# Kernel tuning notes

Hardware: AMD Instinct MI355X
Metric: run time of the kernel (lower is better)

## Reference

```python
import jax, jax.numpy as jnp
from jax import lax
import numpy as np

SCALE_N = 4
KERN = 5
PAD = KERN // 2
_G = np.float32([[0.003765, 0.015019, 0.023792, 0.015019, 0.003765],
                 [0.015019, 0.059912, 0.094907, 0.059912, 0.015019],
                 [0.023792, 0.094907, 0.150342, 0.094907, 0.023792],
                 [0.015019, 0.059912, 0.094907, 0.059912, 0.015019],
                 [0.003765, 0.015019, 0.023792, 0.015019, 0.003765]])
FILTER = jnp.asarray(_G)


def _lap_split(img):
    N, c, H, W = img.shape
    f = jnp.broadcast_to(FILTER, (c, 1, KERN, KERN))
    smooth = lax.conv_general_dilated(img, f, (1, 1), [(PAD, PAD), (PAD, PAD)],
                                      feature_group_count=c)
    lo = smooth[:, :, ::2, ::2]
    oph, opw = (H + 1) % 2, (W + 1) % 2
    # conv_transpose2d(stride=2, padding=PAD, output_padding) as lhs-dilated conv
    # (Gaussian kernel is symmetric, so no spatial flip needed)
    lo2 = 4.0 * lax.conv_general_dilated(
        lo, f, (1, 1),
        [(KERN - 1 - PAD, KERN - 1 - PAD + oph), (KERN - 1 - PAD, KERN - 1 - PAD + opw)],
        lhs_dilation=(2, 2), feature_group_count=c)
    hi = img - lo2
    return lo, hi


def _pyramid(img):
    levels = []
    for _ in range(SCALE_N):
        img, hi = _lap_split(img)
        levels.append(hi)
    levels.append(img)
    return levels


def _sample_points(img, xs, ys):
    # bilinear grid_sample, align_corners=False, zero padding.
    # img: (N,C,H,W); xs, ys: (P,) normalized coords in [-1,1]. -> (N,C,P)
    N, C, H, W = img.shape
    fx = ((xs + 1.0) * W - 1.0) * 0.5
    fy = ((ys + 1.0) * H - 1.0) * 0.5
    x0 = jnp.floor(fx)
    y0 = jnp.floor(fy)
    wx = fx - x0
    wy = fy - y0
    x0i = x0.astype(jnp.int32)
    y0i = y0.astype(jnp.int32)
    out = jnp.zeros((N, C, xs.shape[0]), img.dtype)
    corners = [(0, 0, (1 - wx) * (1 - wy)), (1, 0, wx * (1 - wy)),
               (0, 1, (1 - wx) * wy), (1, 1, wx * wy)]
    for dx, dy, w in corners:
        xc = x0i + dx
        yc = y0i + dy
        valid = (xc >= 0) & (xc < W) & (yc >= 0) & (yc < H)
        xcc = jnp.clip(xc, 0, W - 1)
        ycc = jnp.clip(yc, 0, H - 1)
        vals = img[:, :, ycc, xcc]  # (N,C,P) gather
        out = out + vals * (w * valid)[None, None, :]
    return out


def setup_inputs() -> dict:
    key = jax.random.key(0)
    k1, k2, k3 = jax.random.split(key, 3)
    N, c, H, W = 64, 32, 128, 128
    outdims = 4096
    m = SCALE_N + 1
    x = jax.random.normal(k1, (N, c, H, W), dtype=jnp.float32)
    grid = jax.random.uniform(k2, (1, outdims, 1, 2), minval=-0.1, maxval=0.1,
                              dtype=jnp.float32)
    features = (jnp.full((1, m * c, 1, outdims), 1.0 / c, jnp.float32)
                + 0.01 * jax.random.normal(k3, (1, m * c, 1, outdims), jnp.float32))
    bias = jnp.zeros((outdims,), jnp.float32)
    return {"x": x, "grid": grid, "features": features, "bias": bias}


def reference(x, grid, features, bias):
    N, c, H, W = x.shape
    m = SCALE_N + 1
    outdims = grid.shape[1]
    g = jnp.clip(grid, -1.0, 1.0)
    xs = g[0, :, 0, 0]  # width coord
    ys = g[0, :, 0, 1]  # height coord
    levels = _pyramid(x)
    pools = [_sample_points(lv, xs, ys) for lv in levels]  # each (N,c,P)
    y = jnp.concatenate(pools, axis=1)  # (N, m*c, P)
    feat = features.reshape(1, m * c, outdims)
    y = (y * feat).sum(axis=1)  # (N, P)
    return y + bias
```

## Files before the change

kernel.cpp:

```cpp
#include <hip/hip_runtime.h>
#include <hip/hip_fp16.h>


#define P1 66
#define P2 34
#define P3 18
#define P4 10
#define OFF_LO1 0
#define OFF_LO2 4224
#define OFF_LO3 5312
#define OFF_LO4 5600
#define SLOT    5680
#define SLOT4   1420

#define G_A 0.0613609f
#define G_B 0.2447700f
#define G_C 0.3877386f

#define T_FOFF   16384
#define PYR_FOFF 196608
#define PSTRIDE  5696

static __device__ __forceinline__ float clampf(float v, float lo, float hi) {
    return fminf(fmaxf(v, lo), hi);
}
static __device__ __forceinline__ int imin(int a, int b) { return a < b ? a : b; }
static __device__ __forceinline__ int imax(int a, int b) { return a > b ? a : b; }

static __device__ __forceinline__ unsigned int pack_h2(float a, float b) {
    __half ha = __float2half_rn(a), hb = __float2half_rn(b);
    unsigned short ua = *(unsigned short*)&ha, ub = *(unsigned short*)&hb;
    return (unsigned int)ua | ((unsigned int)ub << 16);
}
static __device__ __forceinline__ unsigned int pack_u2(int a, int b) {
    return (unsigned int)(a & 0xffff) | ((unsigned int)b << 16);
}
static __device__ __forceinline__ float2 uph2(unsigned int u) {
    unsigned short lo = (unsigned short)(u & 0xffff), hi = (unsigned short)(u >> 16);
    __half hl = *(__half*)&lo, hh = *(__half*)&hi;
    return make_float2(__half2float(hl), __half2float(hh));
}

__global__ void init_out_kernel(const float* __restrict__ bias, float* __restrict__ y) {
    int i = blockIdx.x * blockDim.x + threadIdx.x;
    y[i] = bias[i & 4095];
}

__global__ void weights_kernel(const float* __restrict__ grid, float* __restrict__ ws) {
    int out = blockIdx.x * blockDim.x + threadIdx.x;
    if (out >= 4096) return;
    float xs = clampf(grid[2 * out + 0], -1.f, 1.f);
    float ys = clampf(grid[2 * out + 1], -1.f, 1.f);

    uint4* L0 = (uint4*)ws;
    uint2* T  = (uint2*)(ws + T_FOFF);

    float fx = (xs + 1.f) * 64.f - 0.5f;
    float fy = (ys + 1.f) * 64.f - 0.5f;
    float x0f = floorf(fx), y0f = floorf(fy);
    int x0 = (int)x0f, y0 = (int)y0f;
    float wx = fx - x0f, wy = fy - y0f;
    float ux0 = (x0 >= 0)      ? (1.f - wx) : 0.f;
    float ux1 = (x0 + 1 < 128) ? wx         : 0.f;
    float uy0 = (y0 >= 0)      ? (1.f - wy) : 0.f;
    float uy1 = (y0 + 1 < 128) ? wy         : 0.f;
    int cx0 = imax(x0, 0), cx1 = imin(x0 + 1, 127);
    int cy0 = imax(y0, 0), cy1 = imin(y0 + 1, 127);
    L0[out] = make_uint4(pack_h2(ux0 * uy0, ux1 * uy0),
                         pack_h2(ux0 * uy1, ux1 * uy1),
                         pack_u2(cy0 * 128 + cx0, cy0 * 128 + cx1),
                         pack_u2(cy1 * 128 + cx0, cy1 * 128 + cx1));

    int   x0p = x0, y0p = y0;
    float ux0p = ux0, ux1p = ux1, uy0p = uy0, uy1p = uy1;

    const int offs[4]    = {OFF_LO1, OFF_LO2, OFF_LO3, OFF_LO4};
    const int strides[4] = {P1, P2, P3, P4};

    for (int j = 1; j <= 4; ++j) {
        const int Wj = 128 >> j, Pj = strides[j - 1], off = offs[j - 1];

        int qx; float a0, a1, a2;
        if (x0p & 1) { qx = (x0p - 1) >> 1;
            a0 = G_B * ux0p + G_A * ux1p; a1 = G_B * ux0p + G_C * ux1p; a2 = G_A * ux1p; }
        else         { qx = (x0p >> 1) - 1;
            a0 = G_A * ux0p; a1 = G_C * ux0p + G_B * ux1p; a2 = G_A * ux0p + G_B * ux1p; }
        int qy; float e0, e1, e2;
        if (y0p & 1) { qy = (y0p - 1) >> 1;
            e0 = G_B * uy0p + G_A * uy1p; e1 = G_B * uy0p + G_C * uy1p; e2 = G_A * uy1p; }
        else         { qy = (y0p >> 1) - 1;
            e0 = G_A * uy0p; e1 = G_C * uy0p + G_B * uy1p; e2 = G_A * uy0p + G_B * uy1p; }

        float half = (float)(Wj >> 1);
        float fxj = (xs + 1.f) * half - 0.5f;
        float fyj = (ys + 1.f) * half - 0.5f;
        float x0jf = floorf(fxj), y0jf = floorf(fyj);
        int x0j = (int)x0jf, y0j = (int)y0jf;
        float wxj = fxj - x0jf, wyj = fyj - y0jf;
        float ux0j = (x0j >= 0)     ? (1.f - wxj) : 0.f;
        float ux1j = (x0j + 1 < Wj) ? wxj         : 0.f;
        float uy0j = (y0j >= 0)     ? (1.f - wyj) : 0.f;
        float uy1j = (y0j + 1 < Wj) ? wyj         : 0.f;

        int bxb = qx & ~1;
        bxb = imin(imax(bxb, 0), Wj - 4);

        float axv[4], bxv[4], ayv[3], byv[3];
        int rv[3];
#pragma unroll
        for (int t = 0; t < 4; ++t) {
            int col = bxb + t;
            int s = col - qx;
            float av = (s == 0) ? a0 : (s == 1) ? a1 : (s == 2) ? a2 : 0.f;
            if (s < 0 || s > 2) av = 0.f;
            int sb = col - x0j;
            float bv = (sb == 0) ? ux0j : (sb == 1) ? ux1j : 0.f;
            axv[t] = av;
            bxv[t] = bv;
        }
#pragma unroll
        for (int t = 0; t < 3; ++t) {
            int row = qy + t;
            bool v = (row >= 0) && (row < Wj);
            float av = (t == 0) ? e0 : (t == 1) ? e1 : e2;
            ayv[t] = v ? av : 0.f;
            int sb = row - y0j;
            byv[t] = (sb == 0) ? uy0j : (sb == 1) ? uy1j : 0.f;
            int rc = imin(imax(row, 0), Wj - 1);
            rv[t] = off + rc * Pj + bxb;
        }

        int tb = (j - 1) * 5 * 4096 + out;
        T[tb]            = make_uint2(pack_h2(axv[0], axv[1]), pack_h2(axv[2], axv[3]));
        T[tb + 4096]     = make_uint2(pack_h2(bxv[0], bxv[1]), pack_h2(bxv[2], bxv[3]));
        T[tb + 2 * 4096] = make_uint2(pack_h2(ayv[0], ayv[1]), pack_h2(ayv[2], 0.f));
        T[tb + 3 * 4096] = make_uint2(pack_h2(byv[0], byv[1]), pack_h2(byv[2], 0.f));
        T[tb + 4 * 4096] = make_uint2(pack_u2(rv[0], rv[1]), pack_u2(rv[2], 0));

        x0p = x0j; y0p = y0j;
        ux0p = ux0j; ux1p = ux1j; uy0p = uy0j; uy1p = uy1j;
    }
}

static __device__ __forceinline__ float down_pt_lds(const float* s, int stride, int S,
                                                    int i, int j) {
    const float g1[5] = {G_A, G_B, G_C, G_B, G_A};
    int by = 2 * i - 2, bx = 2 * j - 2;
    float acc = 0.f;
    if (by >= 0 && by + 4 < S && bx >= 0 && bx + 4 < S) {
#pragma unroll
        for (int dy = 0; dy < 5; ++dy) {
            const float* r = s + (by + dy) * stride + bx;
            acc += g1[dy] * (G_A * (r[0] + r[4]) + G_B * (r[1] + r[3]) + G_C * r[2]);
        }
    } else {
#pragma unroll
        for (int dy = 0; dy < 5; ++dy) {
            int yy = by + dy;
            if ((unsigned)yy < (unsigned)S) {
#pragma unroll
                for (int dx = 0; dx < 5; ++dx) {
                    int xx = bx + dx;
                    if ((unsigned)xx < (unsigned)S)
                        acc += g1[dy] * g1[dx] * s[yy * stride + xx];
                }
            }
        }
    }
    return acc;
}

static __device__ __forceinline__ void build_pyramid(const float* __restrict__ img,
                                                     float* __restrict__ s_lo, int tid) {
    const float g1[5] = {G_A, G_B, G_C, G_B, G_A};

    for (int r = tid; r < 1024; r += 256) {
        int i = r >> 4, j0 = (r & 15) << 2;
        int by = 2 * i - 2;
        float acc[4] = {0.f, 0.f, 0.f, 0.f};
        if (i >= 1 && i <= 62 && j0 >= 4 && j0 <= 56) {
            const int a = 2 * j0 - 4;
#pragma unroll
            for (int dy = 0; dy < 5; ++dy) {
                const float* rp = img + (by + dy) * 128 + a;
                float4 q0 = *(const float4*)(rp);
                float4 q1 = *(const float4*)(rp + 4);
                float4 q2 = *(const float4*)(rp + 8);
                float4 q3 = *(const float4*)(rp + 12);
                float s2 = q0.z, s3 = q0.w, s4 = q1.x, s5 = q1.y, s6 = q1.z,
                      s7 = q1.w, s8 = q2.x, s9 = q2.y, s10 = q2.z, s11 = q2.w,
                      s12 = q3.x;
                float g = g1[dy];
                acc[0] += g * (G_A * (s2 + s6)  + G_B * (s3 + s5)  + G_C * s4);
                acc[1] += g * (G_A * (s4 + s8)  + G_B * (s5 + s7)  + G_C * s6);
                acc[2] += g * (G_A * (s6 + s10) + G_B * (s7 + s9)  + G_C * s8);
                acc[3] += g * (G_A * (s8 + s12) + G_B * (s9 + s11) + G_C * s10);
            }
        } else {
            int bx = 2 * j0 - 2;
#pragma unroll
            for (int dy = 0; dy < 5; ++dy) {
                int yy = by + dy;
                if ((unsigned)yy < 128u) {
#pragma unroll
                    for (int t = 0; t < 11; ++t) {
                        int xx = bx + t;
                        if ((unsigned)xx < 128u) {
                            float v = img[yy * 128 + xx];
#pragma unroll
                            for (int jj = 0; jj < 4; ++jj) {
                                int dx = t - 2 * jj;
                                if (dx >= 0 && dx <= 4) acc[jj] += g1[dy] * g1[dx] * v;
                            }
                        }
                    }
                }
            }
        }
        int base = OFF_LO1 + i * P1 + j0;
        *(float2*)&s_lo[base]     = make_float2(acc[0], acc[1]);
        *(float2*)&s_lo[base + 2] = make_float2(acc[2], acc[3]);
    }
    __syncthreads();

    for (int p = tid; p < 1024; p += 256) {
        int i = p >> 5, j = p & 31;
        s_lo[OFF_LO2 + i * P2 + j] = down_pt_lds(s_lo + OFF_LO1, P1, 64, i, j);
    }
    __syncthreads();

    {
        int i = tid >> 4, j = tid & 15;
        s_lo[OFF_LO3 + i * P3 + j] = down_pt_lds(s_lo + OFF_LO2, P2, 32, i, j);
    }
    __syncthreads();

    if (tid < 64) {
        int i = tid >> 3, j = tid & 7;
        s_lo[OFF_LO4 + i * P4 + j] = down_pt_lds(s_lo + OFF_LO3, P3, 16, i, j);
    }
    __syncthreads();
}

__global__ __launch_bounds__(256) void pyr_build_kernel(
    const float* __restrict__ x, float* __restrict__ ws)
{
    __shared__ __align__(16) float s_lo[SLOT];
    const int tid = threadIdx.x;
    const int bid = blockIdx.x;
    const float* img = x + ((size_t)bid << 14);

    build_pyramid(img, s_lo, tid);

    float4* g4 = (float4*)(ws + PYR_FOFF + (size_t)bid * PSTRIDE);
    const float4* s4 = (const float4*)s_lo;
    for (int i = tid; i < SLOT4; i += 256) g4[i] = s4[i];
}

__global__ __launch_bounds__(256) void pyr_gather_kernel(
    const float* __restrict__ x, const float* __restrict__ wrec,
    const float* __restrict__ feat, const float* __restrict__ bias,
    float* __restrict__ y)
{
    __shared__ __align__(16) float s_p[2][PSTRIDE];
    const int tid  = threadIdx.x;
    const int n    = blockIdx.x >> 4;
    const int tile = blockIdx.x & 15;
    const int out  = (tile << 8) + tid;

    const uint4* L0 = (const uint4*)wrec;
    const uint2* T  = (const uint2*)(wrec + T_FOFF);

    uint4 h0 = L0[out];
    float2 wA = uph2(h0.x), wB = uph2(h0.y);
    int o00 = (int)(h0.z & 0xffff), o01 = (int)(h0.z >> 16);
    int o10 = (int)(h0.w & 0xffff), o11 = (int)(h0.w >> 16);

    float ax[4][4], bx[4][4], ay[4][3], by[4][3];
    int   rv[4][3];
#pragma unroll
    for (int j = 0; j < 4; ++j) {
        const int tb = j * 5 * 4096 + out;
        uint2 uAX = T[tb];
        uint2 uBX = T[tb + 4096];
        uint2 uAY = T[tb + 2 * 4096];
        uint2 uBY = T[tb + 3 * 4096];
        uint2 uR  = T[tb + 4 * 4096];
        float2 t;
        t = uph2(uAX.x); ax[j][0] = t.x; ax[j][1] = t.y;
        t = uph2(uAX.y); ax[j][2] = t.x; ax[j][3] = t.y;
        t = uph2(uBX.x); bx[j][0] = t.x; bx[j][1] = t.y;
        t = uph2(uBX.y); bx[j][2] = t.x; bx[j][3] = t.y;
        t = uph2(uAY.x); ay[j][0] = t.x; ay[j][1] = t.y;
        ay[j][2] = uph2(uAY.y).x;
        t = uph2(uBY.x); by[j][0] = t.x; by[j][1] = t.y;
        by[j][2] = uph2(uBY.y).x;
        rv[j][0] = (int)(uR.x & 0xffff);
        rv[j][1] = (int)(uR.x >> 16);
        rv[j][2] = (int)(uR.y & 0xffff);
    }

    const float* img_n = x + ((size_t)n << 19);
    const float* pyr_n = wrec + PYR_FOFF + (size_t)n * 32 * PSTRIDE;

    {
        const float4* g = (const float4*)pyr_n;
        float4* d = (float4*)s_p[0];
        for (int i = tid; i < SLOT4; i += 256) d[i] = g[i];
    }
    __syncthreads();

    float acc = 0.f;
#pragma unroll 1
    for (int c = 0; c < 32; ++c) {
        const int cur = c & 1;

        float4 st0, st1, st2, st3, st4, st5;
        const bool have_next = (c + 1 < 32);
        if (have_next) {
            const float4* g = (const float4*)(pyr_n + (size_t)(c + 1) * PSTRIDE);
            int i0 = tid;
            st0 = g[i0];
            st1 = g[i0 + 256];
            st2 = g[i0 + 512];
            st3 = g[i0 + 768];
            st4 = g[i0 + 1024];
            st5 = (i0 + 1280 < SLOT4) ? g[i0 + 1280] : make_float4(0.f, 0.f, 0.f, 0.f);
        }

        const float* sl  = s_p[cur];
        const float* img = img_n + ((size_t)c << 14);
        float f_prev = feat[((size_t)c << 12) + out];
        float v0 = wA.x * img[o00] + wA.y * img[o01] + wB.x * img[o10] + wB.y * img[o11];
        float a = f_prev * v0;

#pragma unroll
        for (int j = 0; j < 4; ++j) {
            float f_cur = feat[((size_t)((j + 1) * 32 + c) << 12) + out];
            int r0 = rv[j][0], r1 = rv[j][1], r2 = rv[j][2];
            float2 p0a = *(const float2*)(sl + r0);
            float2 p0b = *(const float2*)(sl + r0 + 2);
            float2 p1a = *(const float2*)(sl + r1);
            float2 p1b = *(const float2*)(sl + r1 + 2);
            float2 p2a = *(const float2*)(sl + r2);
            float2 p2b = *(const float2*)(sl + r2 + 2);
            float ra0 = ax[j][0] * p0a.x + ax[j][1] * p0a.y + ax[j][2] * p0b.x + ax[j][3] * p0b.y;
            float ra1 = ax[j][0] * p1a.x + ax[j][1] * p1a.y + ax[j][2] * p1b.x + ax[j][3] * p1b.y;
            float ra2 = ax[j][0] * p2a.x + ax[j][1] * p2a.y + ax[j][2] * p2b.x + ax[j][3] * p2b.y;
            float rb0 = bx[j][0] * p0a.x + bx[j][1] * p0a.y + bx[j][2] * p0b.x + bx[j][3] * p0b.y;
            float rb1 = bx[j][0] * p1a.x + bx[j][1] * p1a.y + bx[j][2] * p1b.x + bx[j][3] * p1b.y;
            float rb2 = bx[j][0] * p2a.x + bx[j][1] * p2a.y + bx[j][2] * p2b.x + bx[j][3] * p2b.y;
            float sa = ay[j][0] * ra0 + ay[j][1] * ra1 + ay[j][2] * ra2;
            float sb = by[j][0] * rb0 + by[j][1] * rb1 + by[j][2] * rb2;
            a += f_cur * sb - 4.f * f_prev * sa;
            f_prev = f_cur;
        }
        acc += a;

        if (have_next) {
            float4* d = (float4*)s_p[cur ^ 1];
            int i0 = tid;
            d[i0]        = st0;
            d[i0 + 256]  = st1;
            d[i0 + 512]  = st2;
            d[i0 + 768]  = st3;
            d[i0 + 1024] = st4;
            if (i0 + 1280 < SLOT4) d[i0 + 1280] = st5;
        }
        __syncthreads();
    }

    y[((size_t)n << 12) + out] = acc + bias[out];
}

__global__ __launch_bounds__(256, 3) void pyr_sample_fused(
    const float* __restrict__ x, const float* __restrict__ wrec,
    const float* __restrict__ feat, float* __restrict__ y)
{
    __shared__ __align__(16) float s_lo[SLOT];
    const int tid = threadIdx.x;
    const int n   = blockIdx.x >> 5;
    const int c   = blockIdx.x & 31;
    const float* img = x + ((size_t)(n * 32 + c) << 14);

    build_pyramid(img, s_lo, tid);

    const uint4* L0 = (const uint4*)wrec;
    const uint2* T  = (const uint2*)(wrec + T_FOFF);
    float* yrow = y + ((size_t)n << 12);
    for (int out = tid; out < 4096; out += 256) {
        uint4 h0 = L0[out];
        float2 wA = uph2(h0.x), wB = uph2(h0.y);
        int o00 = (int)(h0.z & 0xffff), o01 = (int)(h0.z >> 16);
        int o10 = (int)(h0.w & 0xffff), o11 = (int)(h0.w >> 16);

        float f_prev = feat[((size_t)c << 12) + out];
        float v0 = wA.x * img[o00] + wA.y * img[o01] + wB.x * img[o10] + wB.y * img[o11];
        float acc = f_prev * v0;

#pragma unroll
        for (int j = 1; j <= 4; ++j) {
            const int tb = (j - 1) * 5 * 4096 + out;
            uint2 uAX = T[tb];
            uint2 uBX = T[tb + 4096];
            uint2 uAY = T[tb + 2 * 4096];
            uint2 uBY = T[tb + 3 * 4096];
            uint2 uR  = T[tb + 4 * 4096];
            float2 ax01 = uph2(uAX.x), ax23 = uph2(uAX.y);
            float2 bx01 = uph2(uBX.x), bx23 = uph2(uBX.y);
            float2 ay01 = uph2(uAY.x); float ay2 = uph2(uAY.y).x;
            float2 by01 = uph2(uBY.x); float by2 = uph2(uBY.y).x;
            int r0 = (int)(uR.x & 0xffff), r1 = (int)(uR.x >> 16), r2 = (int)(uR.y & 0xffff);

            float f_cur = feat[((size_t)(j * 32 + c) << 12) + out];

            float2 p0a = *(const float2*)&s_lo[r0];
            float2 p0b = *(const float2*)&s_lo[r0 + 2];
            float2 p1a = *(const float2*)&s_lo[r1];
            float2 p1b = *(const float2*)&s_lo[r1 + 2];
            float2 p2a = *(const float2*)&s_lo[r2];
            float2 p2b = *(const float2*)&s_lo[r2 + 2];
            float ra0 = ax01.x * p0a.x + ax01.y * p0a.y + ax23.x * p0b.x + ax23.y * p0b.y;
            float ra1 = ax01.x * p1a.x + ax01.y * p1a.y + ax23.x * p1b.x + ax23.y * p1b.y;
            float ra2 = ax01.x * p2a.x + ax01.y * p2a.y + ax23.x * p2b.x + ax23.y * p2b.y;
            float rb0 = bx01.x * p0a.x + bx01.y * p0a.y + bx23.x * p0b.x + bx23.y * p0b.y;
            float rb1 = bx01.x * p1a.x + bx01.y * p1a.y + bx23.x * p1b.x + bx23.y * p1b.y;
            float rb2 = bx01.x * p2a.x + bx01.y * p2a.y + bx23.x * p2b.x + bx23.y * p2b.y;
            float sa = ay01.x * ra0 + ay01.y * ra1 + ay2 * ra2;
            float sb = by01.x * rb0 + by01.y * rb1 + by2 * rb2;
            acc += f_cur * sb - 4.f * f_prev * sa;
            f_prev = f_cur;
        }
        atomicAdd(&yrow[out], acc);
    }
}

extern "C" void kernel_launch(void* const* d_in, const int* in_sizes, int n_in,
                              void* d_out, int out_size, void* d_ws, size_t ws_size,
                              hipStream_t stream) {
    (void)in_sizes; (void)n_in;
    const float* x    = (const float*)d_in[0];
    const float* grid = (const float*)d_in[1];
    const float* feat = (const float*)d_in[2];
    const float* bias = (const float*)d_in[3];
    float* y  = (float*)d_out;
    float* ws = (float*)d_ws;

    const size_t NEED = sizeof(float) * ((size_t)PYR_FOFF + 2048ull * PSTRIDE);

    weights_kernel<<<16, 256, 0, stream>>>(grid, ws);
    if (ws_size >= NEED) {
        pyr_build_kernel<<<2048, 256, 0, stream>>>(x, ws);
        pyr_gather_kernel<<<1024, 256, 0, stream>>>(x, ws, feat, bias, y);
    } else {
        init_out_kernel<<<out_size / 256, 256, 0, stream>>>(bias, y);
        pyr_sample_fused<<<2048, 256, 0, stream>>>(x, ws, feat, y);
    }
}
```

Measured before the change: 365.3 us.

## Compute 4 output rows per thread in level-1 blur with separable row reuse

Each thread now computes a 4x4 block of the first downsampled level instead of looping over 1x4 quads. It does the horizontal 5-tap filter once per input row and reuses it across the vertical taps of the four output rows, so an 11-row window is read instead of 20. The gather kernel's block index is also swizzled to change the order in which images and tiles are scheduled across CUs. The cost is more accumulator registers per thread, which may lower occupancy.

```diff
diff --git a/kernel.cpp b/kernel.cpp
--- a/kernel.cpp
+++ b/kernel.cpp
@@ -170,56 +170,81 @@
     return acc;
 }
 
-static __device__ __forceinline__ void build_pyramid(const float* __restrict__ img,
-                                                     float* __restrict__ s_lo, int tid) {
+static __device__ __forceinline__ void border_quad(const float* __restrict__ img,
+                                                   int i, int j0, float acc[4]) {
     const float g1[5] = {G_A, G_B, G_C, G_B, G_A};
-
-    for (int r = tid; r < 1024; r += 256) {
-        int i = r >> 4, j0 = (r & 15) << 2;
-        int by = 2 * i - 2;
-        float acc[4] = {0.f, 0.f, 0.f, 0.f};
-        if (i >= 1 && i <= 62 && j0 >= 4 && j0 <= 56) {
+    int by = 2 * i - 2, bx = 2 * j0 - 2;
+#pragma unroll
+    for (int dy = 0; dy < 5; ++dy) {
+        int yy = by + dy;
+        if ((unsigned)yy < 128u) {
+#pragma unroll
+            for (int t = 0; t < 11; ++t) {
+                int xx = bx + t;
+                if ((unsigned)xx < 128u) {
+                    float v = img[yy * 128 + xx];
+#pragma unroll
+                    for (int jj = 0; jj < 4; ++jj) {
+                        int dx = t - 2 * jj;
+                        if (dx >= 0 && dx <= 4) acc[jj] += g1[dy] * g1[dx] * v;
+                    }
+                }
+            }
+        }
+    }
+}
+
+static __device__ __forceinline__ void build_pyramid1(const float* __restrict__ img,
+                                                      float* __restrict__ s_lo, int tid) {
+    const float g1[5] = {G_A, G_B, G_C, G_B, G_A};
+
+    {
+        const int jq = tid & 15;
+        const int s  = tid >> 4;
+        const int j0 = jq << 2;
+        float acc[4][4] = {{0.f,0.f,0.f,0.f},{0.f,0.f,0.f,0.f},
+                           {0.f,0.f,0.f,0.f},{0.f,0.f,0.f,0.f}};
+        if (jq >= 1 && jq <= 14) {
             const int a = 2 * j0 - 4;
-#pragma unroll
-            for (int dy = 0; dy < 5; ++dy) {
-                const float* rp = img + (by + dy) * 128 + a;
-                float4 q0 = *(const float4*)(rp);
-                float4 q1 = *(const float4*)(rp + 4);
-                float4 q2 = *(const float4*)(rp + 8);
-                float4 q3 = *(const float4*)(rp + 12);
-                float s2 = q0.z, s3 = q0.w, s4 = q1.x, s5 = q1.y, s6 = q1.z,
-                      s7 = q1.w, s8 = q2.x, s9 = q2.y, s10 = q2.z, s11 = q2.w,
-                      s12 = q3.x;
-                float g = g1[dy];
-                acc[0] += g * (G_A * (s2 + s6)  + G_B * (s3 + s5)  + G_C * s4);
-                acc[1] += g * (G_A * (s4 + s8)  + G_B * (s5 + s7)  + G_C * s6);
-                acc[2] += g * (G_A * (s6 + s10) + G_B * (s7 + s9)  + G_C * s8);
-                acc[3] += g * (G_A * (s8 + s12) + G_B * (s9 + s11) + G_C * s10);
-            }
-        } else {
-            int bx = 2 * j0 - 2;
-#pragma unroll
-            for (int dy = 0; dy < 5; ++dy) {
-                int yy = by + dy;
-                if ((unsigned)yy < 128u) {
-#pragma unroll
-                    for (int t = 0; t < 11; ++t) {
-                        int xx = bx + t;
-                        if ((unsigned)xx < 128u) {
-                            float v = img[yy * 128 + xx];
-#pragma unroll
-                            for (int jj = 0; jj < 4; ++jj) {
-                                int dx = t - 2 * jj;
-                                if (dx >= 0 && dx <= 4) acc[jj] += g1[dy] * g1[dx] * v;
-                            }
+            const int ybase = 8 * s - 2;
+#pragma unroll
+            for (int t5 = 0; t5 < 11; ++t5) {
+                int y = ybase + t5;
+                if ((unsigned)y < 128u) {
+                    const float* rp = img + y * 128 + a;
+                    float4 q0 = *(const float4*)(rp);
+                    float4 q1 = *(const float4*)(rp + 4);
+                    float4 q2 = *(const float4*)(rp + 8);
+                    float4 q3 = *(const float4*)(rp + 12);
+                    float s2 = q0.z, s3 = q0.w, s4 = q1.x, s5 = q1.y, s6 = q1.z,
+                          s7 = q1.w, s8 = q2.x, s9 = q2.y, s10 = q2.z, s11 = q2.w,
+                          s12 = q3.x;
+                    float h0 = G_A * (s2 + s6)  + G_B * (s3 + s5)  + G_C * s4;
+                    float h1 = G_A * (s4 + s8)  + G_B * (s5 + s7)  + G_C * s6;
+                    float h2 = G_A * (s6 + s10) + G_B * (s7 + s9)  + G_C * s8;
+                    float h3 = G_A * (s8 + s12) + G_B * (s9 + s11) + G_C * s10;
+#pragma unroll
+                    for (int k = 0; k < 4; ++k) {
+                        int dy = t5 - 2 * k;
+                        if (dy >= 0 && dy <= 4) {
+                            float g = g1[dy];
+                            acc[k][0] += g * h0; acc[k][1] += g * h1;
+                            acc[k][2] += g * h2; acc[k][3] += g * h3;
                         }
                     }
                 }
             }
-        }
-        int base = OFF_LO1 + i * P1 + j0;
-        *(float2*)&s_lo[base]     = make_float2(acc[0], acc[1]);
-        *(float2*)&s_lo[base + 2] = make_float2(acc[2], acc[3]);
+        } else {
+#pragma unroll
+            for (int k = 0; k < 4; ++k)
+                border_quad(img, 4 * s + k, j0, acc[k]);
+        }
+#pragma unroll
+        for (int k = 0; k < 4; ++k) {
+            int base = OFF_LO1 + (4 * s + k) * P1 + j0;
+            *(float2*)&s_lo[base]     = make_float2(acc[k][0], acc[k][1]);
+            *(float2*)&s_lo[base + 2] = make_float2(acc[k][2], acc[k][3]);
+        }
     }
     __syncthreads();
 
@@ -250,7 +275,7 @@
     const int bid = blockIdx.x;
     const float* img = x + ((size_t)bid << 14);
 
-    build_pyramid(img, s_lo, tid);
+    build_pyramid1(img, s_lo, tid);
 
     float4* g4 = (float4*)(ws + PYR_FOFF + (size_t)bid * PSTRIDE);
     const float4* s4 = (const float4*)s_lo;
@@ -264,8 +289,10 @@
 {
     __shared__ __align__(16) float s_p[2][PSTRIDE];
     const int tid  = threadIdx.x;
-    const int n    = blockIdx.x >> 4;
-    const int tile = blockIdx.x & 15;
+    const int bid  = blockIdx.x;
+    const int sw   = ((bid & 7) << 7) | (bid >> 3);
+    const int n    = sw >> 4;
+    const int tile = sw & 15;
     const int out  = (tile << 8) + tid;
 
     const uint4* L0 = (const uint4*)wrec;
@@ -383,7 +410,7 @@
     const int c   = blockIdx.x & 31;
     const float* img = x + ((size_t)(n * 32 + c) << 14);
 
-    build_pyramid(img, s_lo, tid);
+    build_pyramid1(img, s_lo, tid);
 
     const uint4* L0 = (const uint4*)wrec;
     const uint2* T  = (const uint2*)(wrec + T_FOFF);
```

New measurement: 344.7 us. 5.6% less time.
